# Kernel tuning notes

Hardware: AMD Instinct MI355X
Metric: run time of the kernel (lower is better)

The kernel has to match this reference:

```python
import jax, jax.numpy as jnp
import numpy as np
import math

_B, _L, _D, _H = 4, 2048, 512, 8
_DH = _D // _H


def setup_inputs() -> dict:
    key = jax.random.key(0)
    ks = jax.random.split(key, 16)
    w_scale = 1.0 / math.sqrt(_D)
    def lin(kw, kb):
        W = jax.random.uniform(kw, (_D, _D), jnp.float32, -w_scale, w_scale)
        b = jax.random.uniform(kb, (_D,), jnp.float32, -w_scale, w_scale)
        return W, b
    Wq_w, Wq_b = lin(ks[0], ks[1])
    Wk_w, Wk_b = lin(ks[2], ks[3])
    Wv_w, Wv_b = lin(ks[4], ks[5])
    fc_w, fc_b = lin(ks[6], ks[7])
    Q = jax.random.normal(ks[8], (_B, _L, _D), jnp.float32)
    K = jax.random.normal(ks[9], (_B, _L, _D), jnp.float32)
    V = jax.random.normal(ks[10], (_B, _L, _D), jnp.float32)
    # E = torch.rand(L, DH): uniform [0,1), non-trainable buffer
    E = jax.random.uniform(ks[11], (_L, _DH), jnp.float32)
    # causal mask: True (1) where attention is disallowed -> gets -1e9
    mask = jnp.triu(jnp.ones((_L, _L), dtype=bool), k=1)[None, None]  # (1,1,L,L)
    return {"Q": Q, "K": K, "V": V, "mask": mask,
            "Wq_w": Wq_w, "Wq_b": Wq_b, "Wk_w": Wk_w, "Wk_b": Wk_b,
            "Wv_w": Wv_w, "Wv_b": Wv_b, "fc_w": fc_w, "fc_b": fc_b,
            "E": E, "H": _H}


def reference(Q, K, V, mask, Wq_w, Wq_b, Wk_w, Wk_b, Wv_w, Wv_b, fc_w, fc_b, E, H):
    B, Lq, D = Q.shape
    DH = D // H

    def proj(x, W, b):  # torch Linear: x @ W.T + b, then split heads -> (B,H,L,DH)
        y = x @ W.T + b
        return y.reshape(B, -1, H, DH).transpose(0, 2, 1, 3)

    q = proj(Q, Wq_w, Wq_b)
    k = proj(K, Wk_w, Wk_b)
    v = proj(V, Wv_w, Wv_b)
    Lk = k.shape[2]

    # _get_left_embedding: last Lq rows of E
    Eu = E[max(0, E.shape[0] - Lq):, :]            # (e, DH), e == Lq here
    e = Eu.shape[0]

    QE = jnp.einsum('bhld,ed->bhle', q, Eu)        # (B,H,Lq,e)
    # _qe_masking: keep QE[..., i, j] where j >= e-1-i (upper anti-triangle)
    i = jnp.arange(Lq)[:, None]
    j = jnp.arange(e)[None, :]
    keep = (i + j >= e - 1).astype(QE.dtype)
    QE = QE * keep

    # _skewing: pad one zero column, reshape, drop first row
    padded = jnp.pad(QE, ((0, 0), (0, 0), (0, 0), (1, 0)))   # (B,H,Lq,e+1)
    Srel = padded.reshape(B, H, e + 1, Lq)[:, :, 1:, :]      # (B,H,e,Lq)
    if Lk < Lq:
        Srel = Srel[:, :, :, :Lk]

    logits = (jnp.einsum('bhld,bhmd->bhlm', q, k) + Srel) / math.sqrt(DH)
    logits = logits + mask.astype(jnp.float32) * (-1e9)
    AW = jax.nn.softmax(logits, axis=-1)
    out = jnp.einsum('bhlm,bhmd->bhld', AW, v)               # (B,H,Lq,DH)
    out = out.transpose(0, 2, 1, 3).reshape(B, -1, D)        # (B,Lq,D)
    return out @ fc_w.T + fc_b
```

## Files before the change

### kernel.cpp

```cpp
#include <hip/hip_runtime.h>
#include <stdint.h>

typedef __bf16 bf16;
typedef float f32x4 __attribute__((ext_vector_type(4)));
typedef bf16 bf16x8 __attribute__((ext_vector_type(8)));
typedef bf16 bf16x4 __attribute__((ext_vector_type(4)));

#define MFMA16(a, b, c) __builtin_amdgcn_mfma_f32_16x16x32_bf16((a), (b), (c), 0, 0, 0)
#define EXP2F(x) __builtin_amdgcn_exp2f(x)

__device__ __forceinline__ void gll16(const void* g, void* l) {
  __builtin_amdgcn_global_load_lds((const __attribute__((address_space(1))) void*)g,
                                   (__attribute__((address_space(3))) void*)l, 16, 0, 0);
}

__global__ __launch_bounds__(256) void convert_all(
    const float4* __restrict__ Q, const float4* __restrict__ K, const float4* __restrict__ V,
    const float4* __restrict__ Wq, const float4* __restrict__ Wk, const float4* __restrict__ Wv,
    const float4* __restrict__ fcw, const float4* __restrict__ E,
    bf16x4* __restrict__ Xq, bf16x4* __restrict__ Xk, bf16x4* __restrict__ Xv,
    bf16x4* __restrict__ Wqb, bf16x4* __restrict__ Wkb, bf16x4* __restrict__ Wvb,
    bf16x4* __restrict__ fcb, bf16x4* __restrict__ Eb) {
  int i = blockIdx.x * 256 + threadIdx.x;
  const float4* s;
  bf16x4* d;
  int off;
  if (i < 1048576) { s = Q; d = Xq; off = i; }
  else if (i < 2097152) { s = K; d = Xk; off = i - 1048576; }
  else if (i < 3145728) { s = V; d = Xv; off = i - 2097152; }
  else if (i < 3211264) { s = Wq; d = Wqb; off = i - 3145728; }
  else if (i < 3276800) { s = Wk; d = Wkb; off = i - 3211264; }
  else if (i < 3342336) { s = Wv; d = Wvb; off = i - 3276800; }
  else if (i < 3407872) { s = fcw; d = fcb; off = i - 3342336; }
  else { s = E; d = Eb; off = i - 3407872; }
  float4 v = s[off];
  bf16x4 o;
  o[0] = (bf16)v.x; o[1] = (bf16)v.y; o[2] = (bf16)v.z; o[3] = (bf16)v.w;
  d[off] = o;
}

__device__ __forceinline__ void gemm_core(const bf16* __restrict__ A, const bf16* __restrict__ Bt,
                                          bf16* ldsA, bf16* ldsB, int m0, int n0,
                                          f32x4 acc[4][4]) {
  const int t = threadIdx.x;
  const int lane = t & 63, w = t >> 6;
  const int l15 = lane & 15, quad = lane >> 4;
  const int wm = w >> 1, wn = w & 1;
#pragma unroll
  for (int i = 0; i < 4; i++)
#pragma unroll
    for (int j = 0; j < 4; j++) acc[i][j] = (f32x4){0.f, 0.f, 0.f, 0.f};

  const int ch0 = t, ch1 = t + 256;
  const int r0 = ch0 >> 2, c0 = (ch0 & 3) ^ (r0 & 3);
  const int r1 = ch1 >> 2, c1 = (ch1 & 3) ^ (r1 & 3);

  int aoff[4], boff[4];
#pragma unroll
  for (int mt = 0; mt < 4; mt++) {
    int m = wm * 64 + mt * 16 + l15;
    aoff[mt] = (m << 6) + ((quad ^ (l15 & 3)) << 4);
    int n = wn * 64 + mt * 16 + l15;
    boff[mt] = (n << 6) + ((quad ^ (l15 & 3)) << 4);
  }
  bf16* ldsA1 = ldsA + w * 512;
  bf16* ldsA2 = ldsA + 2048 + w * 512;
  bf16* ldsB1 = ldsB + w * 512;
  bf16* ldsB2 = ldsB + 2048 + w * 512;

  for (int kt = 0; kt < 512; kt += 32) {
    gll16(A + (size_t)(m0 + r0) * 512 + kt + c0 * 8, ldsA1);
    gll16(A + (size_t)(m0 + r1) * 512 + kt + c1 * 8, ldsA2);
    gll16(Bt + (size_t)(n0 + r0) * 512 + kt + c0 * 8, ldsB1);
    gll16(Bt + (size_t)(n0 + r1) * 512 + kt + c1 * 8, ldsB2);
    __syncthreads();
    bf16x8 af[4], bfr[4];
#pragma unroll
    for (int mt = 0; mt < 4; mt++) af[mt] = *(const bf16x8*)((const char*)ldsA + aoff[mt]);
#pragma unroll
    for (int nt = 0; nt < 4; nt++) bfr[nt] = *(const bf16x8*)((const char*)ldsB + boff[nt]);
#pragma unroll
    for (int mt = 0; mt < 4; mt++)
#pragma unroll
      for (int nt = 0; nt < 4; nt++)
        acc[mt][nt] = MFMA16(af[mt], bfr[nt], acc[mt][nt]);
    __syncthreads();
  }
}

__global__ __launch_bounds__(256) void proj_gemm(
    const bf16* __restrict__ Xq, const bf16* __restrict__ Xk, const bf16* __restrict__ Xv,
    const bf16* __restrict__ Wq, const bf16* __restrict__ Wk, const bf16* __restrict__ Wv,
    const float* __restrict__ bq, const float* __restrict__ bk, const float* __restrict__ bv,
    bf16* __restrict__ qb, bf16* __restrict__ kb, bf16* __restrict__ vb) {
  __shared__ bf16 ldsA[128 * 32];
  __shared__ bf16 ldsB[128 * 32];
  const int z = blockIdx.z;
  const bf16* A = z == 0 ? Xq : (z == 1 ? Xk : Xv);
  const bf16* W = z == 0 ? Wq : (z == 1 ? Wk : Wv);
  const float* bias = z == 0 ? bq : (z == 1 ? bk : bv);
  bf16* out = z == 0 ? qb : (z == 1 ? kb : vb);
  const int m0 = blockIdx.x * 128, n0 = blockIdx.y * 128;
  f32x4 acc[4][4];
  gemm_core(A, W, ldsA, ldsB, m0, n0, acc);

  const int t = threadIdx.x;
  const int lane = t & 63, w = t >> 6;
  const int l15 = lane & 15, quad = lane >> 4;
  const int wm = w >> 1, wn = w & 1;
#pragma unroll
  for (int mt = 0; mt < 4; mt++)
#pragma unroll
    for (int nt = 0; nt < 4; nt++)
#pragma unroll
      for (int r = 0; r < 4; r++) {
        int gm = m0 + wm * 64 + mt * 16 + quad * 4 + r;
        int gn = n0 + wn * 64 + nt * 16 + l15;
        float v = acc[mt][nt][r] + bias[gn];
        int b = gm >> 11, l = gm & 2047, h = gn >> 6, d = gn & 63;
        out[(((size_t)(b * 8 + h)) * 2048 + l) * 64 + d] = (bf16)v;
      }
}

__global__ __launch_bounds__(256) void final_gemm(const bf16* __restrict__ A,
                                                  const bf16* __restrict__ W,
                                                  const float* __restrict__ bias,
                                                  float* __restrict__ out) {
  __shared__ bf16 ldsA[128 * 32];
  __shared__ bf16 ldsB[128 * 32];
  const int m0 = blockIdx.x * 128, n0 = blockIdx.y * 128;
  f32x4 acc[4][4];
  gemm_core(A, W, ldsA, ldsB, m0, n0, acc);

  const int t = threadIdx.x;
  const int lane = t & 63, w = t >> 6;
  const int l15 = lane & 15, quad = lane >> 4;
  const int wm = w >> 1, wn = w & 1;
#pragma unroll
  for (int mt = 0; mt < 4; mt++)
#pragma unroll
    for (int nt = 0; nt < 4; nt++)
#pragma unroll
      for (int r = 0; r < 4; r++) {
        int gm = m0 + wm * 64 + mt * 16 + quad * 4 + r;
        int gn = n0 + wn * 64 + nt * 16 + l15;
        out[(size_t)gm * 512 + gn] = acc[mt][nt][r] + bias[gn];
      }
}

__global__ __launch_bounds__(256) void transpose_v(const bf16* __restrict__ vbuf,
                                                   bf16* __restrict__ vT) {
  __shared__ bf16 tile[64][72];
  const int bh = blockIdx.y, l0 = blockIdx.x * 64;
  const bf16* src = vbuf + ((size_t)bh * 2048 + l0) * 64;
  bf16* dst = vT + (size_t)bh * 64 * 2048 + l0;
  const int t = threadIdx.x;
#pragma unroll
  for (int p = 0; p < 2; p++) {
    int ch = t + p * 256;
    int r = ch >> 3, c8 = ch & 7;
    *(bf16x8*)&tile[r][c8 * 8] = *(const bf16x8*)&src[(size_t)r * 64 + c8 * 8];
  }
  __syncthreads();
#pragma unroll
  for (int p = 0; p < 2; p++) {
    int ch = t + p * 256;
    int dr = ch >> 3, lc = ch & 7;
    bf16x8 v;
#pragma unroll
    for (int j = 0; j < 8; j++) v[j] = tile[lc * 8 + j][dr];
    *(bf16x8*)&dst[(size_t)dr * 2048 + lc * 8] = v;
  }
}

__global__ __launch_bounds__(256, 4) void attn_kernel(
    const bf16* __restrict__ qbuf, const bf16* __restrict__ kbuf,
    const bf16* __restrict__ vT, const bf16* __restrict__ Eb,
    bf16* __restrict__ attnb, bf16* __restrict__ Of1,
    float* __restrict__ Os0, float* __restrict__ Os1) {
  __shared__ bf16 Kl[64 * 64];
  __shared__ bf16 Vl[64 * 64];
  __shared__ bf16 Pl[4][16 * 72];
  const int t = threadIdx.x, w = t >> 6, lane = t & 63;
  const int l15 = lane & 15, quad = lane >> 4;
  const int x = blockIdx.x;
  const int bh = x & 31, job = x >> 5;
  int strip, jt0, jt1;
  bool isB;
  if (job < 16) {
    strip = 16 + job; jt0 = 0; jt1 = 16; isB = false;
  } else {
    int k = job - 16, i = k >> 1;
    if ((k & 1) == 0) { strip = 15 - i; jt0 = 0; jt1 = 16 - i; isB = false; }
    else { strip = 31 - i; jt0 = 16; jt1 = 32 - i; isB = true; }
  }
  const int i0 = strip * 64 + w * 16;
  bf16* Pw = Pl[w];
  const bf16* qh = qbuf + (size_t)bh * 2048 * 64;
  const bf16* kh = kbuf + (size_t)bh * 2048 * 64;
  const bf16* vh = vT + (size_t)bh * 64 * 2048;

  const int sr0 = t >> 3, sc0 = (t & 7) ^ (sr0 & 7);
  const int sr1 = sr0 + 32;
  const int wb0 = (t & 192) * 16;
  const int wb1 = 4096 + wb0;

  int bpaddr[4];
  bool loA[4];
#pragma unroll
  for (int r = 0; r < 4; r++) {
    int u = quad * 4 + r;
    bpaddr[r] = (((l15 + 15 - u) & 15) + 16 * quad) * 4;
    loA[r] = (l15 <= u);
  }

  bf16x8 aq0, aq1;
  {
    const bf16* qrow = qh + (size_t)(i0 + l15) * 64 + quad * 8;
    aq0 = *(const bf16x8*)qrow;
    aq1 = *(const bf16x8*)(qrow + 32);
  }
  bf16x8 ones;
#pragma unroll
  for (int j = 0; j < 8; j++) ones[j] = (bf16)1.0f;

  f32x4 O[4], Osum;
  Osum = (f32x4){0.f, 0.f, 0.f, 0.f};
#pragma unroll
  for (int i = 0; i < 4; i++) O[i] = (f32x4){0.f, 0.f, 0.f, 0.f};
  const float sc = 0.125f * 1.44269504088896f;
  const int ebase00 = 2047 - i0 - 15;

  float Bpc[4];
  {
    int er = ebase00 + jt0 * 64 + l15;
    er = er > 2047 ? 2047 : er;
    const bf16* erow = Eb + (size_t)er * 64 + quad * 8;
    bf16x8 e0 = *(const bf16x8*)erow;
    bf16x8 e1 = *(const bf16x8*)(erow + 32);
    f32x4 zz = (f32x4){0.f, 0.f, 0.f, 0.f};
    zz = MFMA16(aq0, e0, zz);
    zz = MFMA16(aq1, e1, zz);
#pragma unroll
    for (int r = 0; r < 4; r++)
      Bpc[r] = __int_as_float(__builtin_amdgcn_ds_bpermute(bpaddr[r], __float_as_int(zz[r])));
  }

  for (int jt = jt0; jt < jt1; jt++) {
    const int j0 = jt * 64;
    const bool diag = (jt == strip);
    __syncthreads();
    gll16(kh + (size_t)(j0 + sr0) * 64 + sc0 * 8, (char*)Kl + wb0);
    gll16(kh + (size_t)(j0 + sr1) * 64 + sc0 * 8, (char*)Kl + wb1);
    gll16(vh + (size_t)sr0 * 2048 + j0 + sc0 * 8, (char*)Vl + wb0);
    gll16(vh + (size_t)sr1 * 2048 + j0 + sc0 * 8, (char*)Vl + wb1);
    float Bp[5][4];
#pragma unroll
    for (int r = 0; r < 4; r++) Bp[0][r] = Bpc[r];
    const int ebase = ebase00 + j0;
#pragma unroll
    for (int nt = 1; nt < 5; nt++) {
      int er = ebase + nt * 16 + l15;
      er = er > 2047 ? 2047 : er;
      const bf16* erow = Eb + (size_t)er * 64 + quad * 8;
      bf16x8 e0 = *(const bf16x8*)erow;
      bf16x8 e1 = *(const bf16x8*)(erow + 32);
      f32x4 zz = (f32x4){0.f, 0.f, 0.f, 0.f};
      zz = MFMA16(aq0, e0, zz);
      zz = MFMA16(aq1, e1, zz);
#pragma unroll
      for (int r = 0; r < 4; r++)
        Bp[nt][r] =
            __int_as_float(__builtin_amdgcn_ds_bpermute(bpaddr[r], __float_as_int(zz[r])));
    }
#pragma unroll
    for (int r = 0; r < 4; r++) Bpc[r] = Bp[4][r];

    __syncthreads();
    f32x4 s[4];
#pragma unroll
    for (int nt = 0; nt < 4; nt++) {
      int row = nt * 16 + l15;
      bf16x8 k0 = *(const bf16x8*)(Kl + ((row << 3) + (quad ^ (row & 7))) * 8);
      bf16x8 k1 = *(const bf16x8*)(Kl + ((row << 3) + ((quad + 4) ^ (row & 7))) * 8);
      f32x4 zz = (f32x4){0.f, 0.f, 0.f, 0.f};
      zz = MFMA16(aq0, k0, zz);
      s[nt] = MFMA16(aq1, k1, zz);
    }
    if (diag) {
#pragma unroll
      for (int nt = 0; nt < 4; nt++)
#pragma unroll
        for (int r = 0; r < 4; r++) {
          int u = quad * 4 + r;
          int j = nt * 16 + l15;
          float skew = loA[r] ? Bp[nt][r] : Bp[nt + 1][r];
          float logit = (s[nt][r] + skew) * sc;
          if (j0 + j > i0 + u) logit = -1e30f;
          Pw[u * 72 + j] = (bf16)EXP2F(logit);
        }
    } else {
#pragma unroll
      for (int nt = 0; nt < 4; nt++)
#pragma unroll
        for (int r = 0; r < 4; r++) {
          int u = quad * 4 + r;
          int j = nt * 16 + l15;
          float skew = loA[r] ? Bp[nt][r] : Bp[nt + 1][r];
          Pw[u * 72 + j] = (bf16)EXP2F((s[nt][r] + skew) * sc);
        }
    }
    bf16x8 pa0 = *(const bf16x8*)&Pw[l15 * 72 + quad * 8];
    bf16x8 pa1 = *(const bf16x8*)&Pw[l15 * 72 + 32 + quad * 8];
    Osum = MFMA16(pa0, ones, Osum);
    Osum = MFMA16(pa1, ones, Osum);
#pragma unroll
    for (int nt = 0; nt < 4; nt++) {
      int row = nt * 16 + l15;
      bf16x8 v0 = *(const bf16x8*)(Vl + ((row << 3) + (quad ^ (row & 7))) * 8);
      bf16x8 v1 = *(const bf16x8*)(Vl + ((row << 3) + ((quad + 4) ^ (row & 7))) * 8);
      O[nt] = MFMA16(pa0, v0, O[nt]);
      O[nt] = MFMA16(pa1, v1, O[nt]);
    }
  }
  if (isB) {
    bf16* orow = Of1 + ((size_t)(bh * 1024 + (i0 - 1024))) * 64;
#pragma unroll
    for (int nt = 0; nt < 4; nt++)
#pragma unroll
      for (int r = 0; r < 4; r++)
        orow[(size_t)(quad * 4 + r) * 64 + nt * 16 + l15] = (bf16)O[nt][r];
    if (l15 == 0) {
#pragma unroll
      for (int r = 0; r < 4; r++) Os1[bh * 1024 + (i0 - 1024) + quad * 4 + r] = Osum[r];
    }
  } else {
    const int b = bh >> 3, hh = bh & 7;
    bf16* orow = attnb + ((size_t)(b * 2048 + i0)) * 512 + hh * 64;
#pragma unroll
    for (int nt = 0; nt < 4; nt++)
#pragma unroll
      for (int r = 0; r < 4; r++)
        orow[(size_t)(quad * 4 + r) * 512 + nt * 16 + l15] = (bf16)O[nt][r];
    if (l15 == 0) {
#pragma unroll
      for (int r = 0; r < 4; r++) Os0[bh * 2048 + i0 + quad * 4 + r] = Osum[r];
    }
  }
}

__global__ __launch_bounds__(256) void norm_kernel(bf16x8* __restrict__ attnb,
                                                   const bf16x8* __restrict__ Of1,
                                                   const float* __restrict__ Os0,
                                                   const float* __restrict__ Os1) {
  int i = blockIdx.x * 256 + threadIdx.x;
  int col8 = i & 63;
  int row = i >> 6;
  int b = row >> 11, l = row & 2047, h = col8 >> 3;
  int bh = b * 8 + h;
  float s = Os0[bh * 2048 + l];
  bf16x8 v0 = attnb[i];
  float acc[8];
#pragma unroll
  for (int j = 0; j < 8; j++) acc[j] = (float)v0[j];
  if (l >= 1024) {
    s += Os1[bh * 1024 + l - 1024];
    bf16x8 v1 = Of1[(size_t)(bh * 1024 + l - 1024) * 8 + (col8 & 7)];
#pragma unroll
    for (int j = 0; j < 8; j++) acc[j] += (float)v1[j];
  }
  float inv = 1.0f / s;
  bf16x8 o;
#pragma unroll
  for (int j = 0; j < 8; j++) o[j] = (bf16)(acc[j] * inv);
  attnb[i] = o;
}

extern "C" void kernel_launch(void* const* d_in, const int* in_sizes, int n_in,
                              void* d_out, int out_size, void* d_ws, size_t ws_size,
                              hipStream_t stream) {
  const float* Q = (const float*)d_in[0];
  const float* K = (const float*)d_in[1];
  const float* V = (const float*)d_in[2];
  const float* Wq = (const float*)d_in[4];
  const float* bq = (const float*)d_in[5];
  const float* Wk = (const float*)d_in[6];
  const float* bk = (const float*)d_in[7];
  const float* Wv = (const float*)d_in[8];
  const float* bv = (const float*)d_in[9];
  const float* fcw = (const float*)d_in[10];
  const float* fcb = (const float*)d_in[11];
  const float* E = (const float*)d_in[12];

  char* ws = (char*)d_ws;
  bf16* Xq = (bf16*)(ws + 0);
  bf16* Xk = (bf16*)(ws + 8388608);
  bf16* Xv = (bf16*)(ws + 16777216);
  bf16* Wqb = (bf16*)(ws + 25165824);
  bf16* Wkb = (bf16*)(ws + 25690112);
  bf16* Wvb = (bf16*)(ws + 26214400);
  bf16* fcwb = (bf16*)(ws + 26738688);
  bf16* Eb = (bf16*)(ws + 27262976);
  bf16* qbuf = (bf16*)(ws + 27525120);
  bf16* kbuf = (bf16*)(ws + 35913728);
  bf16* vbuf = (bf16*)(ws + 44302336);
  bf16* Of1 = (bf16*)(ws + 52690944);
  float* Os0 = (float*)(ws + 56885248);
  float* Os1 = (float*)(ws + 57147392);
  bf16* vTb = Xk;
  bf16* attnb = Xq;

  convert_all<<<13440, 256, 0, stream>>>(
      (const float4*)Q, (const float4*)K, (const float4*)V, (const float4*)Wq,
      (const float4*)Wk, (const float4*)Wv, (const float4*)fcw, (const float4*)E,
      (bf16x4*)Xq, (bf16x4*)Xk, (bf16x4*)Xv, (bf16x4*)Wqb, (bf16x4*)Wkb,
      (bf16x4*)Wvb, (bf16x4*)fcwb, (bf16x4*)Eb);

  proj_gemm<<<dim3(64, 4, 3), 256, 0, stream>>>(Xq, Xk, Xv, Wqb, Wkb, Wvb, bq, bk, bv,
                                                qbuf, kbuf, vbuf);

  transpose_v<<<dim3(32, 32), 256, 0, stream>>>(vbuf, vTb);

  attn_kernel<<<1536, 256, 0, stream>>>(qbuf, kbuf, vTb, Eb, attnb, Of1, Os0, Os1);

  norm_kernel<<<2048, 256, 0, stream>>>((bf16x8*)attnb, (const bf16x8*)Of1, Os0, Os1);

  final_gemm<<<dim3(64, 4, 1), 256, 0, stream>>>(attnb, fcwb, fcb, (float*)d_out);
}
```

Measured before the change: 247.9 us.

## Fuse V transpose into projection epilogue and register-prefetch K/V tiles in attention

The V projection epilogue now writes its output directly in transposed (d-major) layout as 4-element bf16 vectors, so the separate transpose_v kernel and its extra round trip through memory are removed. In the attention loop, the async global-to-LDS loads are replaced with register prefetch: the next K/V tile is loaded into registers while the current one is processed, then stored to LDS at the top of the next iteration. The relative-position skew terms for the next tile are computed after the softmax step so they overlap with the PV MFMAs. s_setprio hints are placed around the MFMA sections. The cost is higher register pressure under the 4-waves launch bound, and the transposed V store is a strided write.

```diff
diff --git a/kernel.cpp b/kernel.cpp
--- a/kernel.cpp
+++ b/kernel.cpp
@@ -92,14 +92,13 @@
     const bf16* __restrict__ Xq, const bf16* __restrict__ Xk, const bf16* __restrict__ Xv,
     const bf16* __restrict__ Wq, const bf16* __restrict__ Wk, const bf16* __restrict__ Wv,
     const float* __restrict__ bq, const float* __restrict__ bk, const float* __restrict__ bv,
-    bf16* __restrict__ qb, bf16* __restrict__ kb, bf16* __restrict__ vb) {
+    bf16* __restrict__ qb, bf16* __restrict__ kb, bf16* __restrict__ vTb) {
   __shared__ bf16 ldsA[128 * 32];
   __shared__ bf16 ldsB[128 * 32];
   const int z = blockIdx.z;
   const bf16* A = z == 0 ? Xq : (z == 1 ? Xk : Xv);
   const bf16* W = z == 0 ? Wq : (z == 1 ? Wk : Wv);
   const float* bias = z == 0 ? bq : (z == 1 ? bk : bv);
-  bf16* out = z == 0 ? qb : (z == 1 ? kb : vb);
   const int m0 = blockIdx.x * 128, n0 = blockIdx.y * 128;
   f32x4 acc[4][4];
   gemm_core(A, W, ldsA, ldsB, m0, n0, acc);
@@ -108,18 +107,35 @@
   const int lane = t & 63, w = t >> 6;
   const int l15 = lane & 15, quad = lane >> 4;
   const int wm = w >> 1, wn = w & 1;
-#pragma unroll
-  for (int mt = 0; mt < 4; mt++)
-#pragma unroll
-    for (int nt = 0; nt < 4; nt++)
-#pragma unroll
-      for (int r = 0; r < 4; r++) {
-        int gm = m0 + wm * 64 + mt * 16 + quad * 4 + r;
+  if (z == 2) {
+#pragma unroll
+    for (int mt = 0; mt < 4; mt++)
+#pragma unroll
+      for (int nt = 0; nt < 4; nt++) {
+        int gm0 = m0 + wm * 64 + mt * 16 + quad * 4;
         int gn = n0 + wn * 64 + nt * 16 + l15;
-        float v = acc[mt][nt][r] + bias[gn];
-        int b = gm >> 11, l = gm & 2047, h = gn >> 6, d = gn & 63;
-        out[(((size_t)(b * 8 + h)) * 2048 + l) * 64 + d] = (bf16)v;
+        int b = gm0 >> 11, l = gm0 & 2047, h = gn >> 6, d = gn & 63;
+        float bi = bias[gn];
+        bf16x4 pv;
+#pragma unroll
+        for (int r = 0; r < 4; r++) pv[r] = (bf16)(acc[mt][nt][r] + bi);
+        *(bf16x4*)&vTb[((size_t)((b * 8 + h) * 64 + d)) * 2048 + l] = pv;
       }
+  } else {
+    bf16* out = z == 0 ? qb : kb;
+#pragma unroll
+    for (int mt = 0; mt < 4; mt++)
+#pragma unroll
+      for (int nt = 0; nt < 4; nt++)
+#pragma unroll
+        for (int r = 0; r < 4; r++) {
+          int gm = m0 + wm * 64 + mt * 16 + quad * 4 + r;
+          int gn = n0 + wn * 64 + nt * 16 + l15;
+          float v = acc[mt][nt][r] + bias[gn];
+          int b = gm >> 11, l = gm & 2047, h = gn >> 6, d = gn & 63;
+          out[(((size_t)(b * 8 + h)) * 2048 + l) * 64 + d] = (bf16)v;
+        }
+  }
 }
 
 __global__ __launch_bounds__(256) void final_gemm(const bf16* __restrict__ A,
@@ -146,31 +162,6 @@
         int gn = n0 + wn * 64 + nt * 16 + l15;
         out[(size_t)gm * 512 + gn] = acc[mt][nt][r] + bias[gn];
       }
-}
-
-__global__ __launch_bounds__(256) void transpose_v(const bf16* __restrict__ vbuf,
-                                                   bf16* __restrict__ vT) {
-  __shared__ bf16 tile[64][72];
-  const int bh = blockIdx.y, l0 = blockIdx.x * 64;
-  const bf16* src = vbuf + ((size_t)bh * 2048 + l0) * 64;
-  bf16* dst = vT + (size_t)bh * 64 * 2048 + l0;
-  const int t = threadIdx.x;
-#pragma unroll
-  for (int p = 0; p < 2; p++) {
-    int ch = t + p * 256;
-    int r = ch >> 3, c8 = ch & 7;
-    *(bf16x8*)&tile[r][c8 * 8] = *(const bf16x8*)&src[(size_t)r * 64 + c8 * 8];
-  }
-  __syncthreads();
-#pragma unroll
-  for (int p = 0; p < 2; p++) {
-    int ch = t + p * 256;
-    int dr = ch >> 3, lc = ch & 7;
-    bf16x8 v;
-#pragma unroll
-    for (int j = 0; j < 8; j++) v[j] = tile[lc * 8 + j][dr];
-    *(bf16x8*)&dst[(size_t)dr * 2048 + lc * 8] = v;
-  }
 }
 
 __global__ __launch_bounds__(256, 4) void attn_kernel(
@@ -202,8 +193,6 @@
 
   const int sr0 = t >> 3, sc0 = (t & 7) ^ (sr0 & 7);
   const int sr1 = sr0 + 32;
-  const int wb0 = (t & 192) * 16;
-  const int wb1 = 4096 + wb0;
 
   int bpaddr[4];
   bool loA[4];
@@ -212,6 +201,15 @@
     int u = quad * 4 + r;
     bpaddr[r] = (((l15 + 15 - u) & 15) + 16 * quad) * 4;
     loA[r] = (l15 <= u);
+  }
+
+  bf16x8 sK0, sK1, sV0, sV1;
+  {
+    int j0 = jt0 * 64;
+    sK0 = *(const bf16x8*)(kh + (size_t)(j0 + sr0) * 64 + sc0 * 8);
+    sK1 = *(const bf16x8*)(kh + (size_t)(j0 + sr1) * 64 + sc0 * 8);
+    sV0 = *(const bf16x8*)(vh + (size_t)sr0 * 2048 + j0 + sc0 * 8);
+    sV1 = *(const bf16x8*)(vh + (size_t)sr1 * 2048 + j0 + sc0 * 8);
   }
 
   bf16x8 aq0, aq1;
@@ -231,9 +229,10 @@
   const float sc = 0.125f * 1.44269504088896f;
   const int ebase00 = 2047 - i0 - 15;
 
-  float Bpc[4];
-  {
-    int er = ebase00 + jt0 * 64 + l15;
+  float Bc[5][4];
+#pragma unroll
+  for (int nt = 0; nt < 5; nt++) {
+    int er = ebase00 + jt0 * 64 + nt * 16 + l15;
     er = er > 2047 ? 2047 : er;
     const bf16* erow = Eb + (size_t)er * 64 + quad * 8;
     bf16x8 e0 = *(const bf16x8*)erow;
@@ -243,40 +242,28 @@
     zz = MFMA16(aq1, e1, zz);
 #pragma unroll
     for (int r = 0; r < 4; r++)
-      Bpc[r] = __int_as_float(__builtin_amdgcn_ds_bpermute(bpaddr[r], __float_as_int(zz[r])));
+      Bc[nt][r] =
+          __int_as_float(__builtin_amdgcn_ds_bpermute(bpaddr[r], __float_as_int(zz[r])));
   }
 
   for (int jt = jt0; jt < jt1; jt++) {
     const int j0 = jt * 64;
     const bool diag = (jt == strip);
+    const bool more = (jt + 1 < jt1);
     __syncthreads();
-    gll16(kh + (size_t)(j0 + sr0) * 64 + sc0 * 8, (char*)Kl + wb0);
-    gll16(kh + (size_t)(j0 + sr1) * 64 + sc0 * 8, (char*)Kl + wb1);
-    gll16(vh + (size_t)sr0 * 2048 + j0 + sc0 * 8, (char*)Vl + wb0);
-    gll16(vh + (size_t)sr1 * 2048 + j0 + sc0 * 8, (char*)Vl + wb1);
-    float Bp[5][4];
-#pragma unroll
-    for (int r = 0; r < 4; r++) Bp[0][r] = Bpc[r];
-    const int ebase = ebase00 + j0;
-#pragma unroll
-    for (int nt = 1; nt < 5; nt++) {
-      int er = ebase + nt * 16 + l15;
-      er = er > 2047 ? 2047 : er;
-      const bf16* erow = Eb + (size_t)er * 64 + quad * 8;
-      bf16x8 e0 = *(const bf16x8*)erow;
-      bf16x8 e1 = *(const bf16x8*)(erow + 32);
-      f32x4 zz = (f32x4){0.f, 0.f, 0.f, 0.f};
-      zz = MFMA16(aq0, e0, zz);
-      zz = MFMA16(aq1, e1, zz);
-#pragma unroll
-      for (int r = 0; r < 4; r++)
-        Bp[nt][r] =
-            __int_as_float(__builtin_amdgcn_ds_bpermute(bpaddr[r], __float_as_int(zz[r])));
-    }
-#pragma unroll
-    for (int r = 0; r < 4; r++) Bpc[r] = Bp[4][r];
-
+    *(bf16x8*)((char*)Kl + t * 16) = sK0;
+    *(bf16x8*)((char*)Kl + 4096 + t * 16) = sK1;
+    *(bf16x8*)((char*)Vl + t * 16) = sV0;
+    *(bf16x8*)((char*)Vl + 4096 + t * 16) = sV1;
+    if (more) {
+      int jn = j0 + 64;
+      sK0 = *(const bf16x8*)(kh + (size_t)(jn + sr0) * 64 + sc0 * 8);
+      sK1 = *(const bf16x8*)(kh + (size_t)(jn + sr1) * 64 + sc0 * 8);
+      sV0 = *(const bf16x8*)(vh + (size_t)sr0 * 2048 + jn + sc0 * 8);
+      sV1 = *(const bf16x8*)(vh + (size_t)sr1 * 2048 + jn + sc0 * 8);
+    }
     __syncthreads();
+    __builtin_amdgcn_s_setprio(1);
     f32x4 s[4];
 #pragma unroll
     for (int nt = 0; nt < 4; nt++) {
@@ -287,6 +274,7 @@
       zz = MFMA16(aq0, k0, zz);
       s[nt] = MFMA16(aq1, k1, zz);
     }
+    __builtin_amdgcn_s_setprio(0);
     if (diag) {
 #pragma unroll
       for (int nt = 0; nt < 4; nt++)
@@ -294,7 +282,7 @@
         for (int r = 0; r < 4; r++) {
           int u = quad * 4 + r;
           int j = nt * 16 + l15;
-          float skew = loA[r] ? Bp[nt][r] : Bp[nt + 1][r];
+          float skew = loA[r] ? Bc[nt][r] : Bc[nt + 1][r];
           float logit = (s[nt][r] + skew) * sc;
           if (j0 + j > i0 + u) logit = -1e30f;
           Pw[u * 72 + j] = (bf16)EXP2F(logit);
@@ -306,12 +294,34 @@
         for (int r = 0; r < 4; r++) {
           int u = quad * 4 + r;
           int j = nt * 16 + l15;
-          float skew = loA[r] ? Bp[nt][r] : Bp[nt + 1][r];
+          float skew = loA[r] ? Bc[nt][r] : Bc[nt + 1][r];
           Pw[u * 72 + j] = (bf16)EXP2F((s[nt][r] + skew) * sc);
         }
     }
+    float carry[4];
+#pragma unroll
+    for (int r = 0; r < 4; r++) carry[r] = Bc[4][r];
     bf16x8 pa0 = *(const bf16x8*)&Pw[l15 * 72 + quad * 8];
     bf16x8 pa1 = *(const bf16x8*)&Pw[l15 * 72 + 32 + quad * 8];
+    if (more) {
+      const int ebn = ebase00 + j0 + 64;
+#pragma unroll
+      for (int nt = 1; nt < 5; nt++) {
+        int er = ebn + nt * 16 + l15;
+        er = er > 2047 ? 2047 : er;
+        const bf16* erow = Eb + (size_t)er * 64 + quad * 8;
+        bf16x8 e0 = *(const bf16x8*)erow;
+        bf16x8 e1 = *(const bf16x8*)(erow + 32);
+        f32x4 zz = (f32x4){0.f, 0.f, 0.f, 0.f};
+        zz = MFMA16(aq0, e0, zz);
+        zz = MFMA16(aq1, e1, zz);
+#pragma unroll
+        for (int r = 0; r < 4; r++)
+          Bc[nt][r] =
+              __int_as_float(__builtin_amdgcn_ds_bpermute(bpaddr[r], __float_as_int(zz[r])));
+      }
+    }
+    __builtin_amdgcn_s_setprio(1);
     Osum = MFMA16(pa0, ones, Osum);
     Osum = MFMA16(pa1, ones, Osum);
 #pragma unroll
@@ -321,6 +331,11 @@
       bf16x8 v1 = *(const bf16x8*)(Vl + ((row << 3) + ((quad + 4) ^ (row & 7))) * 8);
       O[nt] = MFMA16(pa0, v0, O[nt]);
       O[nt] = MFMA16(pa1, v1, O[nt]);
+    }
+    __builtin_amdgcn_s_setprio(0);
+    if (more) {
+#pragma unroll
+      for (int r = 0; r < 4; r++) Bc[0][r] = carry[r];
     }
   }
   if (isB) {
@@ -403,11 +418,10 @@
   bf16* Eb = (bf16*)(ws + 27262976);
   bf16* qbuf = (bf16*)(ws + 27525120);
   bf16* kbuf = (bf16*)(ws + 35913728);
-  bf16* vbuf = (bf16*)(ws + 44302336);
+  bf16* vTb = (bf16*)(ws + 44302336);
   bf16* Of1 = (bf16*)(ws + 52690944);
   float* Os0 = (float*)(ws + 56885248);
   float* Os1 = (float*)(ws + 57147392);
-  bf16* vTb = Xk;
   bf16* attnb = Xq;
 
   convert_all<<<13440, 256, 0, stream>>>(
@@ -417,9 +431,7 @@
       (bf16x4*)Wvb, (bf16x4*)fcwb, (bf16x4*)Eb);
 
   proj_gemm<<<dim3(64, 4, 3), 256, 0, stream>>>(Xq, Xk, Xv, Wqb, Wkb, Wvb, bq, bk, bv,
-                                                qbuf, kbuf, vbuf);
-
-  transpose_v<<<dim3(32, 32), 256, 0, stream>>>(vbuf, vTb);
+                                                qbuf, kbuf, vTb);
 
   attn_kernel<<<1536, 256, 0, stream>>>(qbuf, kbuf, vTb, Eb, attnb, Of1, Os0, Os1);
 
```

New measurement: 254.2 us. 1.03x slower.

## Double-buffer K/V tiles and prefetch next-tile skew terms in attention loop

Applied to the files above, without the earlier changes.

Turns the K/V shared-memory tiles into double buffers. The next tile's global-to-LDS loads are issued at the start of each iteration, and the next tile's relative-position (E) MFMA terms are computed between the P and PV stages. This removes one barrier per iteration and lets load latency overlap with compute. It also wraps the MFMA sections in s_setprio. The cost is double the LDS for K/V (about 16KB more per block), which may reduce occupancy under the 4-blocks-per-CU launch bound, plus more live registers for the prefetched skew values.

```diff
diff --git a/kernel.cpp b/kernel.cpp
--- a/kernel.cpp
+++ b/kernel.cpp
@@ -178,8 +178,8 @@
     const bf16* __restrict__ vT, const bf16* __restrict__ Eb,
     bf16* __restrict__ attnb, bf16* __restrict__ Of1,
     float* __restrict__ Os0, float* __restrict__ Os1) {
-  __shared__ bf16 Kl[64 * 64];
-  __shared__ bf16 Vl[64 * 64];
+  __shared__ bf16 Kl[2][64 * 64];
+  __shared__ bf16 Vl[2][64 * 64];
   __shared__ bf16 Pl[4][16 * 72];
   const int t = threadIdx.x, w = t >> 6, lane = t & 63;
   const int l15 = lane & 15, quad = lane >> 4;
@@ -214,6 +214,14 @@
     loA[r] = (l15 <= u);
   }
 
+  {
+    int j0 = jt0 * 64;
+    gll16(kh + (size_t)(j0 + sr0) * 64 + sc0 * 8, (char*)Kl + wb0);
+    gll16(kh + (size_t)(j0 + sr1) * 64 + sc0 * 8, (char*)Kl + wb1);
+    gll16(vh + (size_t)sr0 * 2048 + j0 + sc0 * 8, (char*)Vl + wb0);
+    gll16(vh + (size_t)sr1 * 2048 + j0 + sc0 * 8, (char*)Vl + wb1);
+  }
+
   bf16x8 aq0, aq1;
   {
     const bf16* qrow = qh + (size_t)(i0 + l15) * 64 + quad * 8;
@@ -231,9 +239,10 @@
   const float sc = 0.125f * 1.44269504088896f;
   const int ebase00 = 2047 - i0 - 15;
 
-  float Bpc[4];
-  {
-    int er = ebase00 + jt0 * 64 + l15;
+  float Bc[5][4];
+#pragma unroll
+  for (int nt = 0; nt < 5; nt++) {
+    int er = ebase00 + jt0 * 64 + nt * 16 + l15;
     er = er > 2047 ? 2047 : er;
     const bf16* erow = Eb + (size_t)er * 64 + quad * 8;
     bf16x8 e0 = *(const bf16x8*)erow;
@@ -243,50 +252,40 @@
     zz = MFMA16(aq1, e1, zz);
 #pragma unroll
     for (int r = 0; r < 4; r++)
-      Bpc[r] = __int_as_float(__builtin_amdgcn_ds_bpermute(bpaddr[r], __float_as_int(zz[r])));
-  }
+      Bc[nt][r] =
+          __int_as_float(__builtin_amdgcn_ds_bpermute(bpaddr[r], __float_as_int(zz[r])));
+  }
+
+  __syncthreads();
 
   for (int jt = jt0; jt < jt1; jt++) {
     const int j0 = jt * 64;
     const bool diag = (jt == strip);
-    __syncthreads();
-    gll16(kh + (size_t)(j0 + sr0) * 64 + sc0 * 8, (char*)Kl + wb0);
-    gll16(kh + (size_t)(j0 + sr1) * 64 + sc0 * 8, (char*)Kl + wb1);
-    gll16(vh + (size_t)sr0 * 2048 + j0 + sc0 * 8, (char*)Vl + wb0);
-    gll16(vh + (size_t)sr1 * 2048 + j0 + sc0 * 8, (char*)Vl + wb1);
-    float Bp[5][4];
-#pragma unroll
-    for (int r = 0; r < 4; r++) Bp[0][r] = Bpc[r];
-    const int ebase = ebase00 + j0;
-#pragma unroll
-    for (int nt = 1; nt < 5; nt++) {
-      int er = ebase + nt * 16 + l15;
-      er = er > 2047 ? 2047 : er;
-      const bf16* erow = Eb + (size_t)er * 64 + quad * 8;
-      bf16x8 e0 = *(const bf16x8*)erow;
-      bf16x8 e1 = *(const bf16x8*)(erow + 32);
-      f32x4 zz = (f32x4){0.f, 0.f, 0.f, 0.f};
-      zz = MFMA16(aq0, e0, zz);
-      zz = MFMA16(aq1, e1, zz);
-#pragma unroll
-      for (int r = 0; r < 4; r++)
-        Bp[nt][r] =
-            __int_as_float(__builtin_amdgcn_ds_bpermute(bpaddr[r], __float_as_int(zz[r])));
-    }
-#pragma unroll
-    for (int r = 0; r < 4; r++) Bpc[r] = Bp[4][r];
-
-    __syncthreads();
+    const bool more = (jt + 1 < jt1);
+    const int cur = (jt - jt0) & 1;
+    const bf16* Kc = Kl[cur];
+    const bf16* Vc = Vl[cur];
+    if (more) {
+      int jn = j0 + 64;
+      char* Kn = (char*)Kl[cur ^ 1];
+      char* Vn = (char*)Vl[cur ^ 1];
+      gll16(kh + (size_t)(jn + sr0) * 64 + sc0 * 8, Kn + wb0);
+      gll16(kh + (size_t)(jn + sr1) * 64 + sc0 * 8, Kn + wb1);
+      gll16(vh + (size_t)sr0 * 2048 + jn + sc0 * 8, Vn + wb0);
+      gll16(vh + (size_t)sr1 * 2048 + jn + sc0 * 8, Vn + wb1);
+    }
+    __builtin_amdgcn_s_setprio(1);
     f32x4 s[4];
 #pragma unroll
     for (int nt = 0; nt < 4; nt++) {
       int row = nt * 16 + l15;
-      bf16x8 k0 = *(const bf16x8*)(Kl + ((row << 3) + (quad ^ (row & 7))) * 8);
-      bf16x8 k1 = *(const bf16x8*)(Kl + ((row << 3) + ((quad + 4) ^ (row & 7))) * 8);
+      bf16x8 k0 = *(const bf16x8*)(Kc + ((row << 3) + (quad ^ (row & 7))) * 8);
+      bf16x8 k1 = *(const bf16x8*)(Kc + ((row << 3) + ((quad + 4) ^ (row & 7))) * 8);
       f32x4 zz = (f32x4){0.f, 0.f, 0.f, 0.f};
       zz = MFMA16(aq0, k0, zz);
       s[nt] = MFMA16(aq1, k1, zz);
     }
+    __builtin_amdgcn_s_setprio(0);
     if (diag) {
 #pragma unroll
       for (int nt = 0; nt < 4; nt++)
@@ -294,7 +293,7 @@
         for (int r = 0; r < 4; r++) {
           int u = quad * 4 + r;
           int j = nt * 16 + l15;
-          float skew = loA[r] ? Bp[nt][r] : Bp[nt + 1][r];
+          float skew = loA[r] ? Bc[nt][r] : Bc[nt + 1][r];
           float logit = (s[nt][r] + skew) * sc;
           if (j0 + j > i0 + u) logit = -1e30f;
           Pw[u * 72 + j] = (bf16)EXP2F(logit);
@@ -306,22 +305,50 @@
         for (int r = 0; r < 4; r++) {
           int u = quad * 4 + r;
           int j = nt * 16 + l15;
-          float skew = loA[r] ? Bp[nt][r] : Bp[nt + 1][r];
+          float skew = loA[r] ? Bc[nt][r] : Bc[nt + 1][r];
           Pw[u * 72 + j] = (bf16)EXP2F((s[nt][r] + skew) * sc);
         }
     }
+    float carry[4];
+#pragma unroll
+    for (int r = 0; r < 4; r++) carry[r] = Bc[4][r];
     bf16x8 pa0 = *(const bf16x8*)&Pw[l15 * 72 + quad * 8];
     bf16x8 pa1 = *(const bf16x8*)&Pw[l15 * 72 + 32 + quad * 8];
+    if (more) {
+      const int ebn = ebase00 + j0 + 64;
+#pragma unroll
+      for (int nt = 1; nt < 5; nt++) {
+        int er = ebn + nt * 16 + l15;
+        er = er > 2047 ? 2047 : er;
+        const bf16* erow = Eb + (size_t)er * 64 + quad * 8;
+        bf16x8 e0 = *(const bf16x8*)erow;
+        bf16x8 e1 = *(const bf16x8*)(erow + 32);
+        f32x4 zz = (f32x4){0.f, 0.f, 0.f, 0.f};
+        zz = MFMA16(aq0, e0, zz);
+        zz = MFMA16(aq1, e1, zz);
+#pragma unroll
+        for (int r = 0; r < 4; r++)
+          Bc[nt][r] =
+              __int_as_float(__builtin_amdgcn_ds_bpermute(bpaddr[r], __float_as_int(zz[r])));
+      }
+    }
+    __builtin_amdgcn_s_setprio(1);
     Osum = MFMA16(pa0, ones, Osum);
     Osum = MFMA16(pa1, ones, Osum);
 #pragma unroll
     for (int nt = 0; nt < 4; nt++) {
       int row = nt * 16 + l15;
-      bf16x8 v0 = *(const bf16x8*)(Vl + ((row << 3) + (quad ^ (row & 7))) * 8);
-      bf16x8 v1 = *(const bf16x8*)(Vl + ((row << 3) + ((quad + 4) ^ (row & 7))) * 8);
+      bf16x8 v0 = *(const bf16x8*)(Vc + ((row << 3) + (quad ^ (row & 7))) * 8);
+      bf16x8 v1 = *(const bf16x8*)(Vc + ((row << 3) + ((quad + 4) ^ (row & 7))) * 8);
       O[nt] = MFMA16(pa0, v0, O[nt]);
       O[nt] = MFMA16(pa1, v1, O[nt]);
     }
+    __builtin_amdgcn_s_setprio(0);
+    if (more) {
+#pragma unroll
+      for (int r = 0; r < 4; r++) Bc[0][r] = carry[r];
+    }
+    __syncthreads();
   }
   if (isB) {
     bf16* orow = Of1 + ((size_t)(bh * 1024 + (i0 - 1024))) * 64;
```

Result: slower. 259.8 us (+4.8%).

## Split attention KV range into 8-tile chunks with longest-first job table

Applied to the files above, without the earlier changes.

Each query strip's causal key range is now split into up to four chunks of 8 key tiles, where before the split was two halves. A static job table orders the 2560 blocks longest-first, and the norm kernel merges up to four partial outputs and sums. The goal is better load balance and a shorter tail across CUs. s_setprio is also raised around the MFMA sections. The cost is more partial-result traffic and workspace aliasing: Of1 and Of3 reuse the vbuf and Xv regions.

```diff
diff --git a/kernel.cpp b/kernel.cpp
--- a/kernel.cpp
+++ b/kernel.cpp
@@ -173,27 +173,40 @@
   }
 }
 
+__device__ const unsigned char JOBTAB[80] = {
+    31*4+0, 31*4+1, 31*4+2, 31*4+3,
+    30*4+0, 30*4+1, 30*4+2,  29*4+0, 29*4+1, 29*4+2,
+    28*4+0, 28*4+1, 28*4+2,  27*4+0, 27*4+1, 27*4+2,
+    26*4+0, 26*4+1, 26*4+2,  25*4+0, 25*4+1, 25*4+2,
+    24*4+0, 24*4+1, 24*4+2,  23*4+0, 23*4+1, 23*4+2,
+    22*4+0, 22*4+1,  21*4+0, 21*4+1,  20*4+0, 20*4+1,  19*4+0, 19*4+1,
+    18*4+0, 18*4+1,  17*4+0, 17*4+1,  16*4+0, 16*4+1,  15*4+0, 15*4+1,
+    14*4+0, 13*4+0, 12*4+0, 11*4+0, 10*4+0, 9*4+0, 8*4+0, 7*4+0,
+    30*4+3, 22*4+2, 14*4+1, 6*4+0,
+    29*4+3, 21*4+2, 13*4+1, 5*4+0,
+    28*4+3, 20*4+2, 12*4+1, 4*4+0,
+    27*4+3, 19*4+2, 11*4+1, 3*4+0,
+    26*4+3, 18*4+2, 10*4+1, 2*4+0,
+    25*4+3, 17*4+2, 9*4+1, 1*4+0,
+    24*4+3, 16*4+2, 8*4+1, 0*4+0};
+
 __global__ __launch_bounds__(256, 4) void attn_kernel(
     const bf16* __restrict__ qbuf, const bf16* __restrict__ kbuf,
     const bf16* __restrict__ vT, const bf16* __restrict__ Eb,
-    bf16* __restrict__ attnb, bf16* __restrict__ Of1,
-    float* __restrict__ Os0, float* __restrict__ Os1) {
+    bf16* __restrict__ attnb, bf16* __restrict__ Of1, bf16* __restrict__ Of2,
+    bf16* __restrict__ Of3, float* __restrict__ Os0, float* __restrict__ Os1,
+    float* __restrict__ Os2, float* __restrict__ Os3) {
   __shared__ bf16 Kl[64 * 64];
   __shared__ bf16 Vl[64 * 64];
   __shared__ bf16 Pl[4][16 * 72];
   const int t = threadIdx.x, w = t >> 6, lane = t & 63;
   const int l15 = lane & 15, quad = lane >> 4;
   const int x = blockIdx.x;
-  const int bh = x & 31, job = x >> 5;
-  int strip, jt0, jt1;
-  bool isB;
-  if (job < 16) {
-    strip = 16 + job; jt0 = 0; jt1 = 16; isB = false;
-  } else {
-    int k = job - 16, i = k >> 1;
-    if ((k & 1) == 0) { strip = 15 - i; jt0 = 0; jt1 = 16 - i; isB = false; }
-    else { strip = 31 - i; jt0 = 16; jt1 = 32 - i; isB = true; }
-  }
+  const int bh = x & 31, jb = x >> 5;
+  const int tab = JOBTAB[jb];
+  const int strip = tab >> 2, ck = tab & 3;
+  const int jt0 = ck << 3;
+  const int jt1 = (jt0 + 8 < strip + 1) ? (jt0 + 8) : (strip + 1);
   const int i0 = strip * 64 + w * 16;
   bf16* Pw = Pl[w];
   const bf16* qh = qbuf + (size_t)bh * 2048 * 64;
@@ -277,6 +290,7 @@
     for (int r = 0; r < 4; r++) Bpc[r] = Bp[4][r];
 
     __syncthreads();
+    __builtin_amdgcn_s_setprio(1);
     f32x4 s[4];
 #pragma unroll
     for (int nt = 0; nt < 4; nt++) {
@@ -287,6 +301,7 @@
       zz = MFMA16(aq0, k0, zz);
       s[nt] = MFMA16(aq1, k1, zz);
     }
+    __builtin_amdgcn_s_setprio(0);
     if (diag) {
 #pragma unroll
       for (int nt = 0; nt < 4; nt++)
@@ -312,6 +327,7 @@
     }
     bf16x8 pa0 = *(const bf16x8*)&Pw[l15 * 72 + quad * 8];
     bf16x8 pa1 = *(const bf16x8*)&Pw[l15 * 72 + 32 + quad * 8];
+    __builtin_amdgcn_s_setprio(1);
     Osum = MFMA16(pa0, ones, Osum);
     Osum = MFMA16(pa1, ones, Osum);
 #pragma unroll
@@ -322,9 +338,26 @@
       O[nt] = MFMA16(pa0, v0, O[nt]);
       O[nt] = MFMA16(pa1, v1, O[nt]);
     }
-  }
-  if (isB) {
-    bf16* orow = Of1 + ((size_t)(bh * 1024 + (i0 - 1024))) * 64;
+    __builtin_amdgcn_s_setprio(0);
+  }
+  if (ck == 0) {
+    const int b = bh >> 3, hh = bh & 7;
+    bf16* orow = attnb + ((size_t)(b * 2048 + i0)) * 512 + hh * 64;
+#pragma unroll
+    for (int nt = 0; nt < 4; nt++)
+#pragma unroll
+      for (int r = 0; r < 4; r++)
+        orow[(size_t)(quad * 4 + r) * 512 + nt * 16 + l15] = (bf16)O[nt][r];
+    if (l15 == 0) {
+#pragma unroll
+      for (int r = 0; r < 4; r++) Os0[bh * 2048 + i0 + quad * 4 + r] = Osum[r];
+    }
+  } else {
+    const int rows0 = ck << 9;
+    const int nrows = 2048 - rows0;
+    bf16* Ofk = ck == 1 ? Of1 : (ck == 2 ? Of2 : Of3);
+    float* Osk = ck == 1 ? Os1 : (ck == 2 ? Os2 : Os3);
+    bf16* orow = Ofk + ((size_t)(bh * nrows + (i0 - rows0))) * 64;
 #pragma unroll
     for (int nt = 0; nt < 4; nt++)
 #pragma unroll
@@ -332,42 +365,48 @@
         orow[(size_t)(quad * 4 + r) * 64 + nt * 16 + l15] = (bf16)O[nt][r];
     if (l15 == 0) {
 #pragma unroll
-      for (int r = 0; r < 4; r++) Os1[bh * 1024 + (i0 - 1024) + quad * 4 + r] = Osum[r];
-    }
-  } else {
-    const int b = bh >> 3, hh = bh & 7;
-    bf16* orow = attnb + ((size_t)(b * 2048 + i0)) * 512 + hh * 64;
-#pragma unroll
-    for (int nt = 0; nt < 4; nt++)
-#pragma unroll
-      for (int r = 0; r < 4; r++)
-        orow[(size_t)(quad * 4 + r) * 512 + nt * 16 + l15] = (bf16)O[nt][r];
-    if (l15 == 0) {
-#pragma unroll
-      for (int r = 0; r < 4; r++) Os0[bh * 2048 + i0 + quad * 4 + r] = Osum[r];
-    }
-  }
-}
-
-__global__ __launch_bounds__(256) void norm_kernel(bf16x8* __restrict__ attnb,
-                                                   const bf16x8* __restrict__ Of1,
-                                                   const float* __restrict__ Os0,
-                                                   const float* __restrict__ Os1) {
+      for (int r = 0; r < 4; r++) Osk[bh * nrows + (i0 - rows0) + quad * 4 + r] = Osum[r];
+    }
+  }
+}
+
+__global__ __launch_bounds__(256) void norm_kernel(
+    bf16x8* __restrict__ attnb, const bf16x8* __restrict__ Of1,
+    const bf16x8* __restrict__ Of2, const bf16x8* __restrict__ Of3,
+    const float* __restrict__ Os0, const float* __restrict__ Os1,
+    const float* __restrict__ Os2, const float* __restrict__ Os3) {
   int i = blockIdx.x * 256 + threadIdx.x;
   int col8 = i & 63;
   int row = i >> 6;
   int b = row >> 11, l = row & 2047, h = col8 >> 3;
   int bh = b * 8 + h;
+  int c8 = col8 & 7;
+  int nch = ((l >> 6) + 8) >> 3;
   float s = Os0[bh * 2048 + l];
   bf16x8 v0 = attnb[i];
   float acc[8];
 #pragma unroll
   for (int j = 0; j < 8; j++) acc[j] = (float)v0[j];
-  if (l >= 1024) {
-    s += Os1[bh * 1024 + l - 1024];
-    bf16x8 v1 = Of1[(size_t)(bh * 1024 + l - 1024) * 8 + (col8 & 7)];
+  if (nch > 1) {
+    int r1 = l - 512;
+    s += Os1[bh * 1536 + r1];
+    bf16x8 v1 = Of1[(size_t)(bh * 1536 + r1) * 8 + c8];
 #pragma unroll
     for (int j = 0; j < 8; j++) acc[j] += (float)v1[j];
+  }
+  if (nch > 2) {
+    int r2 = l - 1024;
+    s += Os2[bh * 1024 + r2];
+    bf16x8 v2 = Of2[(size_t)(bh * 1024 + r2) * 8 + c8];
+#pragma unroll
+    for (int j = 0; j < 8; j++) acc[j] += (float)v2[j];
+  }
+  if (nch > 3) {
+    int r3 = l - 1536;
+    s += Os3[bh * 512 + r3];
+    bf16x8 v3 = Of3[(size_t)(bh * 512 + r3) * 8 + c8];
+#pragma unroll
+    for (int j = 0; j < 8; j++) acc[j] += (float)v3[j];
   }
   float inv = 1.0f / s;
   bf16x8 o;
@@ -404,9 +443,13 @@
   bf16* qbuf = (bf16*)(ws + 27525120);
   bf16* kbuf = (bf16*)(ws + 35913728);
   bf16* vbuf = (bf16*)(ws + 44302336);
-  bf16* Of1 = (bf16*)(ws + 52690944);
+  bf16* Of1 = (bf16*)(ws + 44302336);
+  bf16* Of2 = (bf16*)(ws + 52690944);
+  bf16* Of3 = (bf16*)(ws + 16777216);
+  float* Os1 = (float*)(ws + 18874368);
+  float* Os2 = (float*)(ws + 19070976);
+  float* Os3 = (float*)(ws + 19202048);
   float* Os0 = (float*)(ws + 56885248);
-  float* Os1 = (float*)(ws + 57147392);
   bf16* vTb = Xk;
   bf16* attnb = Xq;
 
@@ -421,9 +464,12 @@
 
   transpose_v<<<dim3(32, 32), 256, 0, stream>>>(vbuf, vTb);
 
-  attn_kernel<<<1536, 256, 0, stream>>>(qbuf, kbuf, vTb, Eb, attnb, Of1, Os0, Os1);
-
-  norm_kernel<<<2048, 256, 0, stream>>>((bf16x8*)attnb, (const bf16x8*)Of1, Os0, Os1);
+  attn_kernel<<<2560, 256, 0, stream>>>(qbuf, kbuf, vTb, Eb, attnb, Of1, Of2, Of3,
+                                        Os0, Os1, Os2, Os3);
+
+  norm_kernel<<<2048, 256, 0, stream>>>((bf16x8*)attnb, (const bf16x8*)Of1,
+                                        (const bf16x8*)Of2, (const bf16x8*)Of3,
+                                        Os0, Os1, Os2, Os3);
 
   final_gemm<<<dim3(64, 4, 1), 256, 0, stream>>>(attnb, fcwb, fcb, (float*)d_out);
 }
```

Measured after the change: 250.8 us. No clear change (+1.2%).
